# Kernel optimization log

Hardware: AMD Instinct MI355X
Metric: run time of the kernel (lower is better)

Reference implementation:

```python
import jax, jax.numpy as jnp
import numpy as np

L, H, E, V, BS = 12, 12, 768, 50257, 1024
HS = E // H
EPS = 1e-5


def _ln(x, w, b):
    m = jnp.mean(x, axis=-1, keepdims=True)
    v = jnp.mean(jnp.square(x - m), axis=-1, keepdims=True)
    return (x - m) * jax.lax.rsqrt(v + EPS) * w + b


def setup_inputs() -> dict:
    key = jax.random.key(0)
    ks = jax.random.split(key, 16)
    s = 0.02
    inp = {
        "idx": jax.random.randint(ks[0], (2, 1024), 0, V),
        "wte": jax.random.normal(ks[1], (V, E), jnp.float32) * s,
        "wpe": jax.random.normal(ks[2], (BS, E), jnp.float32) * s,
        "ln1_w": jnp.ones((L, E), jnp.float32),
        "ln1_b": jnp.zeros((L, E), jnp.float32),
        "attn_w": jax.random.normal(ks[3], (L, E, 3 * E), jnp.float32) * s,
        "attn_b": jnp.zeros((L, 3 * E), jnp.float32),
        "proj_w": jax.random.normal(ks[4], (L, E, E), jnp.float32) * s,
        "proj_b": jnp.zeros((L, E), jnp.float32),
        "ln2_w": jnp.ones((L, E), jnp.float32),
        "ln2_b": jnp.zeros((L, E), jnp.float32),
        "fc_w": jax.random.normal(ks[5], (L, E, 4 * E), jnp.float32) * s,
        "fc_b": jnp.zeros((L, 4 * E), jnp.float32),
        "fcp_w": jax.random.normal(ks[6], (L, 4 * E, E), jnp.float32) * s,
        "fcp_b": jnp.zeros((L, E), jnp.float32),
        "lnf_w": jnp.ones((E,), jnp.float32),
        "lnf_b": jnp.zeros((E,), jnp.float32),
    }
    return inp


def _gpt_forward(idx, wte, wpe, ln1_w, ln1_b, attn_w, attn_b, proj_w, proj_b,
                 ln2_w, ln2_b, fc_w, fc_b, fcp_w, fcp_b, lnf_w, lnf_b):
    B, T = idx.shape
    x = wte[idx] + wpe[:T]  # [B,T,E]
    causal = jnp.tril(jnp.ones((T, T), bool))
    scale = 1.0 / np.sqrt(HS)

    def block(x, p):
        (l1w, l1b, aw, ab, pw, pb, l2w, l2b, fw, fb, pww, pwb) = p
        qkv = _ln(x, l1w, l1b) @ aw + ab  # [B,T,3E]
        q, k, v = jnp.split(qkv, 3, axis=-1)
        q = q.reshape(B, T, H, HS).transpose(0, 2, 1, 3)  # [B,H,T,hs]
        k = k.reshape(B, T, H, HS).transpose(0, 2, 1, 3)
        v = v.reshape(B, T, H, HS).transpose(0, 2, 1, 3)
        att = jnp.einsum('bhqd,bhkd->bhqk', q, k) * scale
        att = jnp.where(causal, att, -jnp.inf)
        att = jax.nn.softmax(att, axis=-1)
        y = jnp.einsum('bhqk,bhkd->bhqd', att, v)
        y = y.transpose(0, 2, 1, 3).reshape(B, T, E)
        x = x + y @ pw + pb
        h = jax.nn.gelu(_ln(x, l2w, l2b) @ fw + fb, approximate=False)
        x = x + h @ pww + pwb
        return x, None

    params = (ln1_w, ln1_b, attn_w, attn_b, proj_w, proj_b,
              ln2_w, ln2_b, fc_w, fc_b, fcp_w, fcp_b)
    x, _ = jax.lax.scan(block, x, params)
    x = _ln(x, lnf_w, lnf_b)
    return x @ wte.T  # tied lm_head, training-mode full logits [B,T,V]


def reference(idx, wte, wpe, ln1_w, ln1_b, attn_w, attn_b, proj_w, proj_b,
              ln2_w, ln2_b, fc_w, fc_b, fcp_w, fcp_b, lnf_w, lnf_b):
    return _gpt_forward(idx, wte, wpe, ln1_w, ln1_b, attn_w, attn_b, proj_w,
                        proj_b, ln2_w, ln2_b, fc_w, fc_b, fcp_w, fcp_b,
                        lnf_w, lnf_b)
```

## Files before the change

kernel.cpp:

```cpp
#include <hip/hip_runtime.h>
#include <hip/hip_bf16.h>


typedef __bf16 bf16x8 __attribute__((ext_vector_type(8)));
typedef float f32x4 __attribute__((ext_vector_type(4)));
typedef unsigned int u32x4 __attribute__((ext_vector_type(4)));
typedef unsigned short ushort_t;

__device__ inline unsigned short f2bf(float f) {
    unsigned int u = __float_as_uint(f);
    u += 0x7FFFu + ((u >> 16) & 1u);
    return (unsigned short)(u >> 16);
}
__device__ inline unsigned int pk2(float a, float b) {
    return (unsigned int)f2bf(a) | ((unsigned int)f2bf(b) << 16);
}
__device__ inline float gelu_f(float v) {
    return 0.5f * v * (1.0f + erff(v * 0.70710678118654752f));
}
__device__ inline void gld16(const ushort_t* g, ushort_t* l) {
    __builtin_amdgcn_global_load_lds(
        (const __attribute__((address_space(1))) void*)g,
        (__attribute__((address_space(3))) void*)l, 16, 0, 0);
}
__device__ inline void store_c(float* p, float v) { *p = v; }
__device__ inline void store_c(ushort_t* p, float v) { *p = f2bf(v); }

__global__ __launch_bounds__(192) void embed_kernel(
    const int* __restrict__ idx, const float* __restrict__ wte,
    const float* __restrict__ wpe, float* __restrict__ x) {
    int row = blockIdx.x;
    int t = row & 1023;
    int tok = idx[row];
    const float4* src = (const float4*)(wte + (size_t)tok * 768);
    const float4* pe  = (const float4*)(wpe + (size_t)t * 768);
    float4* dst = (float4*)(x + (size_t)row * 768);
    int i = threadIdx.x;
    float4 a = src[i], b = pe[i];
    float4 r; r.x = a.x + b.x; r.y = a.y + b.y; r.z = a.z + b.z; r.w = a.w + b.w;
    dst[i] = r;
}

__device__ inline void ln_body(
    const float* __restrict__ in, const float* __restrict__ w,
    const float* __restrict__ b, ushort_t* __restrict__ out, int row) {
    const float* r = in + (size_t)row * 768;
    int tid = threadIdx.x;
    float v[3];
#pragma unroll
    for (int j = 0; j < 3; j++) v[j] = r[tid + j * 256];
    float s = v[0] + v[1] + v[2];
    __shared__ float sh1[4], sh2[4];
#pragma unroll
    for (int o = 32; o; o >>= 1) s += __shfl_down(s, o);
    if ((tid & 63) == 0) sh1[tid >> 6] = s;
    __syncthreads();
    float mean = (sh1[0] + sh1[1] + sh1[2] + sh1[3]) * (1.0f / 768.0f);
    float d0 = v[0] - mean, d1 = v[1] - mean, d2 = v[2] - mean;
    float sq = d0 * d0 + d1 * d1 + d2 * d2;
#pragma unroll
    for (int o = 32; o; o >>= 1) sq += __shfl_down(sq, o);
    if ((tid & 63) == 0) sh2[tid >> 6] = sq;
    __syncthreads();
    float var = (sh2[0] + sh2[1] + sh2[2] + sh2[3]) * (1.0f / 768.0f);
    float rstd = rsqrtf(var + 1e-5f);
#pragma unroll
    for (int j = 0; j < 3; j++) {
        int c = tid + j * 256;
        out[(size_t)row * 768 + c] = f2bf((v[j] - mean) * rstd * w[c] + b[c]);
    }
}

__global__ __launch_bounds__(256) void ln_kernel(
    const float* __restrict__ in, const float* __restrict__ w,
    const float* __restrict__ b, ushort_t* __restrict__ out) {
    ln_body(in, w, b, out, blockIdx.x);
}

__device__ inline void transpose_tile(
    const float* __restrict__ in, ushort_t* __restrict__ out,
    int N, int K, int n0, int k0) {
    __shared__ float tl[64][65];
    int tid = threadIdx.x;
    int r = tid >> 4, c = (tid & 15) * 4;
#pragma unroll
    for (int j = 0; j < 4; j++) {
        float4 v = *(const float4*)(in + (size_t)(k0 + r + j * 16) * N + n0 + c);
        tl[r + j * 16][c] = v.x; tl[r + j * 16][c + 1] = v.y;
        tl[r + j * 16][c + 2] = v.z; tl[r + j * 16][c + 3] = v.w;
    }
    __syncthreads();
    int nr = tid >> 2, kc = (tid & 3) * 16;
    unsigned int u[8];
#pragma unroll
    for (int j = 0; j < 8; j++)
        u[j] = pk2(tl[kc + 2 * j][nr], tl[kc + 2 * j + 1][nr]);
    u32x4 a = {u[0], u[1], u[2], u[3]}, b = {u[4], u[5], u[6], u[7]};
    ushort_t* op = out + (size_t)(n0 + nr) * K + k0 + kc;
    *(u32x4*)op = a;
    *(u32x4*)(op + 8) = b;
}

__global__ __launch_bounds__(256) void prep1_kernel(
    const float* __restrict__ aw, const float* __restrict__ pw,
    const float* __restrict__ fw, const float* __restrict__ fpw,
    ushort_t* __restrict__ awT, ushort_t* __restrict__ pwT,
    ushort_t* __restrict__ fwT, ushort_t* __restrict__ fpwT,
    const float* __restrict__ x, const float* __restrict__ lw,
    const float* __restrict__ lb, ushort_t* __restrict__ xn) {
    int t = blockIdx.x;
    if (t >= 1728) { ln_body(x, lw, lb, xn, t - 1728); return; }
    const float* in; ushort_t* out; int N, K, n0, k0;
    if (t < 432)       { in = aw;  out = awT;  N = 2304; K = 768;
                         n0 = (t % 36) * 64; k0 = (t / 36) * 64; }
    else if (t < 576)  { t -= 432;  in = pw;  out = pwT;  N = 768;  K = 768;
                         n0 = (t % 12) * 64; k0 = (t / 12) * 64; }
    else if (t < 1152) { t -= 576;  in = fw;  out = fwT;  N = 3072; K = 768;
                         n0 = (t % 48) * 64; k0 = (t / 48) * 64; }
    else               { t -= 1152; in = fpw; out = fpwT; N = 768;  K = 3072;
                         n0 = (t % 12) * 64; k0 = (t / 12) * 64; }
    transpose_tile(in, out, N, K, n0, k0);
}

__global__ __launch_bounds__(256) void convert_bf(
    const float* __restrict__ in, ushort_t* __restrict__ out, long long n8) {
    long long i = (long long)blockIdx.x * 256 + threadIdx.x;
    long long stride = (long long)gridDim.x * 256;
    for (; i < n8; i += stride) {
        const float4* s = (const float4*)(in + i * 8);
        float4 a = s[0], b = s[1];
        u32x4 u = {pk2(a.x, a.y), pk2(a.z, a.w), pk2(b.x, b.y), pk2(b.z, b.w)};
        *(u32x4*)(out + i * 8) = u;
    }
}

__global__ __launch_bounds__(256) void attn_kernel(
    const ushort_t* __restrict__ qkvb,
    const ushort_t* __restrict__ vt,
    ushort_t* __restrict__ y) {
    int qt = (int)gridDim.x - 1 - (int)blockIdx.x;
    int q0 = qt * 128;
    int z = blockIdx.y;
    int b = z / 12, h = z % 12;

    __shared__ __align__(16) ushort_t Ks[64 * 64];
    __shared__ __align__(16) ushort_t Vs[64 * 64];
    __shared__ __align__(16) ushort_t Ps[4][32 * 72];

    int tid = threadIdx.x;
    int lane = tid & 63, w = tid >> 6;
    int fr = lane & 15;
    int g4 = lane >> 4;
    int kg = g4 * 8;

    const ushort_t* qbase = qkvb + (size_t)b * 1024 * 2304;
    bf16x8 qf[2][2];
#pragma unroll
    for (int m = 0; m < 2; m++)
#pragma unroll
        for (int ks = 0; ks < 2; ks++)
            qf[m][ks] = *(const bf16x8*)(qbase +
                (size_t)(q0 + w * 32 + m * 16 + fr) * 2304 + h * 64 + ks * 32 + kg);

    f32x4 oacc[2][4] = {};
    float mrow[2][4], lrow[2][4];
#pragma unroll
    for (int m = 0; m < 2; m++)
#pragma unroll
        for (int i = 0; i < 4; i++) { mrow[m][i] = -1e30f; lrow[m][i] = 0.f; }

    const ushort_t* vtb = vt + (size_t)z * 64 * 1024;
    int nkt = ((q0 + 127) >> 6) + 1;
    const float LOG2E = 1.4426950408889634f;
    const float sc = 0.125f;
    int swr = (fr & 7) << 3;

    for (int kt = 0; kt < nkt; kt++) {
        int k0 = kt << 6;
#pragma unroll
        for (int c2 = 0; c2 < 2; c2++) {
            int c = tid + c2 * 256;
            int row = c >> 3;
            int col8 = ((c & 7) << 3) ^ ((row & 7) << 3);
            gld16(qbase + (size_t)(k0 + row) * 2304 + 768 + h * 64 + col8, Ks + c * 8);
            gld16(vtb + (size_t)row * 1024 + k0 + col8, Vs + c * 8);
        }
        __syncthreads();
        bool active = (k0 <= q0 + w * 32 + 31);
        if (active) {
            f32x4 s[2][4] = {};
#pragma unroll
            for (int ks = 0; ks < 2; ks++) {
                int cc = (ks * 32 + kg) ^ swr;
                bf16x8 kf[4];
#pragma unroll
                for (int n = 0; n < 4; n++)
                    kf[n] = *(const bf16x8*)(Ks + (n * 16 + fr) * 64 + cc);
#pragma unroll
                for (int m = 0; m < 2; m++)
#pragma unroll
                    for (int n = 0; n < 4; n++)
                        s[m][n] = __builtin_amdgcn_mfma_f32_16x16x32_bf16(qf[m][ks], kf[n], s[m][n], 0, 0, 0);
            }
            float al[2][4];
#pragma unroll
            for (int m = 0; m < 2; m++) {
#pragma unroll
                for (int i = 0; i < 4; i++) {
                    int q = q0 + w * 32 + m * 16 + g4 * 4 + i;
                    float pm = -1e30f;
#pragma unroll
                    for (int n = 0; n < 4; n++) {
                        int kv = k0 + n * 16 + fr;
                        float v = (kv <= q) ? s[m][n][i] * sc : -1e30f;
                        s[m][n][i] = v;
                        pm = fmaxf(pm, v);
                    }
                    pm = fmaxf(pm, __shfl_xor(pm, 1));
                    pm = fmaxf(pm, __shfl_xor(pm, 2));
                    pm = fmaxf(pm, __shfl_xor(pm, 4));
                    pm = fmaxf(pm, __shfl_xor(pm, 8));
                    float mn = fmaxf(mrow[m][i], pm);
                    float alpha = __builtin_exp2f((mrow[m][i] - mn) * LOG2E);
                    mrow[m][i] = mn;
                    al[m][i] = alpha;
                    float ps = 0.f;
#pragma unroll
                    for (int n = 0; n < 4; n++) {
                        float pv = __builtin_exp2f((s[m][n][i] - mn) * LOG2E);
                        s[m][n][i] = pv;
                        ps += pv;
                    }
                    ps += __shfl_xor(ps, 1);
                    ps += __shfl_xor(ps, 2);
                    ps += __shfl_xor(ps, 4);
                    ps += __shfl_xor(ps, 8);
                    lrow[m][i] = lrow[m][i] * alpha + ps;
                }
            }
#pragma unroll
            for (int m = 0; m < 2; m++)
#pragma unroll
                for (int nd = 0; nd < 4; nd++)
#pragma unroll
                    for (int i = 0; i < 4; i++)
                        oacc[m][nd][i] *= al[m][i];
#pragma unroll
            for (int m = 0; m < 2; m++)
#pragma unroll
                for (int n = 0; n < 4; n++)
#pragma unroll
                    for (int i = 0; i < 4; i++)
                        Ps[w][(m * 16 + g4 * 4 + i) * 72 + n * 16 + fr] = f2bf(s[m][n][i]);
        }
        __syncthreads();
        if (active) {
#pragma unroll
            for (int ks = 0; ks < 2; ks++) {
                int cc = (ks * 32 + kg) ^ swr;
                bf16x8 pa[2], vf[4];
#pragma unroll
                for (int m = 0; m < 2; m++)
                    pa[m] = *(const bf16x8*)(&Ps[w][(m * 16 + fr) * 72 + ks * 32 + kg]);
#pragma unroll
                for (int nd = 0; nd < 4; nd++)
                    vf[nd] = *(const bf16x8*)(Vs + (nd * 16 + fr) * 64 + cc);
#pragma unroll
                for (int m = 0; m < 2; m++)
#pragma unroll
                    for (int nd = 0; nd < 4; nd++)
                        oacc[m][nd] = __builtin_amdgcn_mfma_f32_16x16x32_bf16(pa[m], vf[nd], oacc[m][nd], 0, 0, 0);
            }
        }
        __syncthreads();
    }
    ushort_t* yb = y + (size_t)b * 1024 * 768 + h * 64;
#pragma unroll
    for (int m = 0; m < 2; m++)
#pragma unroll
        for (int nd = 0; nd < 4; nd++)
#pragma unroll
            for (int i = 0; i < 4; i++) {
                int q = q0 + w * 32 + m * 16 + g4 * 4 + i;
                yb[(size_t)q * 768 + nd * 16 + fr] = f2bf(oacc[m][nd][i] / lrow[m][i]);
            }
}

template <int BM, int EPI, typename TC>
__global__ __launch_bounds__(256) void gemm2(
    const ushort_t* __restrict__ A, int lda,
    const ushort_t* __restrict__ B, int ldb,
    TC* __restrict__ C, int ldc,
    const float* __restrict__ bias, const float* __restrict__ R,
    ushort_t* __restrict__ VT,
    int M, int N, int K) {
    constexpr int MR = BM / 32;
    int brow = blockIdx.y * BM;
    int bcol = blockIdx.x * 128;

    __shared__ __align__(16) ushort_t As[BM * 64];
    __shared__ __align__(16) ushort_t Bs[128 * 64];
    __shared__ __align__(16) ushort_t Tr[EPI == 3 ? 128 * 80 : 1];

    int tid = threadIdx.x;
    int lane = tid & 63, wid = tid >> 6;
    int wr = (wid >> 1) * (BM / 2);
    int wc = (wid & 1) * 64;
    int fr = lane & 15;
    int g4 = lane >> 4;
    int kg = g4 * 8;
    int swr = (fr & 7) << 3;

    int colk = ((tid & 7) << 3) ^ (((tid >> 3) & 7) << 3);
    const ushort_t* Agr[MR];
    const ushort_t* Bgr[4];
#pragma unroll
    for (int rg = 0; rg < MR; rg++)
        Agr[rg] = A + (size_t)(brow + rg * 32 + (tid >> 3)) * lda + colk;
#pragma unroll
    for (int rg = 0; rg < 4; rg++) {
        int br = bcol + rg * 32 + (tid >> 3);
        if (br > N - 1) br = N - 1;
        Bgr[rg] = B + (size_t)br * ldb + colk;
    }
    ushort_t* Al = As + tid * 8;
    ushort_t* Bl = Bs + tid * 8;

    f32x4 acc[MR][4] = {};

    for (int k0 = 0; k0 < K; k0 += 64) {
#pragma unroll
        for (int rg = 0; rg < MR; rg++) gld16(Agr[rg] + k0, Al + rg * 2048);
#pragma unroll
        for (int rg = 0; rg < 4; rg++) gld16(Bgr[rg] + k0, Bl + rg * 2048);
        __syncthreads();
#pragma unroll
        for (int ks = 0; ks < 2; ks++) {
            int cc = (ks * 32 + kg) ^ swr;
            bf16x8 af[MR], bfv[4];
#pragma unroll
            for (int m = 0; m < MR; m++)
                af[m] = *(const bf16x8*)(As + (wr + m * 16 + fr) * 64 + cc);
#pragma unroll
            for (int n = 0; n < 4; n++)
                bfv[n] = *(const bf16x8*)(Bs + (wc + n * 16 + fr) * 64 + cc);
#pragma unroll
            for (int m = 0; m < MR; m++)
#pragma unroll
                for (int n = 0; n < 4; n++)
                    acc[m][n] = __builtin_amdgcn_mfma_f32_16x16x32_bf16(af[m], bfv[n], acc[m][n], 0, 0, 0);
        }
        __syncthreads();
    }

    int cr = g4 * 4;

    if constexpr (EPI == 3) {
        if (bcol >= 1536) {
#pragma unroll
            for (int m = 0; m < MR; m++) {
#pragma unroll
                for (int n = 0; n < 4; n++) {
                    int dl = wc + n * 16 + fr;
                    float bv = bias[bcol + dl];
#pragma unroll
                    for (int i = 0; i < 4; i++) {
                        int tl = wr + m * 16 + cr + i;
                        Tr[dl * 80 + tl] = f2bf(acc[m][n][i] + bv);
                    }
                }
            }
            __syncthreads();
            int bb = brow >> 10, t0g = brow & 1023;
            int dbase = bcol - 1536;
#pragma unroll
            for (int j = 0; j < 4; j++) {
                int lin = tid + j * 256;
                int dl = lin >> 3, t8 = (lin & 7) * 8;
                int dg = dbase + dl;
                int h2 = dg >> 6, dd = dg & 63;
                u32x4 v = *(const u32x4*)&Tr[dl * 80 + t8];
                *(u32x4*)(VT + ((size_t)(bb * 12 + h2) * 64 + dd) * 1024 + t0g + t8) = v;
            }
            return;
        }
    }

#pragma unroll
    for (int m = 0; m < MR; m++) {
#pragma unroll
        for (int n = 0; n < 4; n++) {
            int col = bcol + wc + n * 16 + fr;
            if (col < N) {
                float bv = bias ? bias[col] : 0.0f;
#pragma unroll
                for (int i = 0; i < 4; i++) {
                    int row = brow + wr + m * 16 + cr + i;
                    float v = acc[m][n][i] + bv;
                    if constexpr (EPI == 1) v = gelu_f(v);
                    if constexpr (EPI == 2) v += R[(size_t)row * ldc + col];
                    store_c(&C[(size_t)row * ldc + col], v);
                }
            }
        }
    }
}

__global__ __launch_bounds__(512, 1) void gemm256(
    const ushort_t* __restrict__ A, int lda,
    const ushort_t* __restrict__ B, int ldb,
    float* __restrict__ C, int ldc,
    int M, int N, int K) {
    int Rt = gridDim.x, P = gridDim.y;
    int wgid = blockIdx.x + Rt * blockIdx.y;
    int full = P >> 3;
    int thresh = full * 8 * Rt;
    int r, pp;
    if (wgid < thresh) {
        int g = wgid / (8 * Rt);
        int wi = wgid - g * (8 * Rt);
        r = wi >> 3;
        pp = g * 8 + (wi & 7);
    } else {
        int off = wgid - thresh;
        pp = full * 8 + off / Rt;
        r = off - (off / Rt) * Rt;
    }
    int brow = r * 256;
    int bcol = pp * 256;

    __shared__ __align__(16) ushort_t As[2][256 * 64];
    __shared__ __align__(16) ushort_t Bs[2][256 * 64];

    int tid = threadIdx.x;
    int lane = tid & 63, wid = tid >> 6;
    int wr = (wid >> 2) * 128;
    int wc = (wid & 3) * 64;
    int fr = lane & 15;
    int g4 = lane >> 4;
    int kg = g4 * 8;
    int swr = (fr & 7) << 3;

    int srow = tid >> 3;
    int scol = ((tid & 7) << 3) ^ ((srow & 7) << 3);
    const ushort_t* Ag[4];
    const ushort_t* Bg[4];
#pragma unroll
    for (int s = 0; s < 4; s++) {
        Ag[s] = A + (size_t)(brow + s * 64 + srow) * lda + scol;
        int br = bcol + s * 64 + srow;
        if (br > N - 1) br = N - 1;
        Bg[s] = B + (size_t)br * ldb + scol;
    }

    f32x4 acc[8][4] = {};
    int nt = K >> 6;

#pragma unroll
    for (int s = 0; s < 4; s++) {
        gld16(Ag[s], &As[0][s * 4096 + tid * 8]);
        gld16(Bg[s], &Bs[0][s * 4096 + tid * 8]);
    }

    for (int t = 0; t < nt; t++) {
        int cur = t & 1;
        if (t + 1 < nt) {
            int nxt = cur ^ 1;
            int k0 = (t + 1) << 6;
#pragma unroll
            for (int s = 0; s < 4; s++) {
                gld16(Ag[s] + k0, &As[nxt][s * 4096 + tid * 8]);
                gld16(Bg[s] + k0, &Bs[nxt][s * 4096 + tid * 8]);
            }
            asm volatile("s_waitcnt vmcnt(8)" ::: "memory");
        } else {
            asm volatile("s_waitcnt vmcnt(0)" ::: "memory");
        }
        __builtin_amdgcn_sched_barrier(0);
        __builtin_amdgcn_s_barrier();
        __builtin_amdgcn_sched_barrier(0);

        const ushort_t* Ab = &As[cur][0];
        const ushort_t* Bb = &Bs[cur][0];
#pragma unroll
        for (int ks = 0; ks < 2; ks++) {
            int cc = (ks * 32 + kg) ^ swr;
            bf16x8 af[8], bfv[4];
#pragma unroll
            for (int m = 0; m < 8; m++)
                af[m] = *(const bf16x8*)(Ab + (wr + m * 16 + fr) * 64 + cc);
#pragma unroll
            for (int n = 0; n < 4; n++)
                bfv[n] = *(const bf16x8*)(Bb + (wc + n * 16 + fr) * 64 + cc);
#pragma unroll
            for (int m = 0; m < 8; m++)
#pragma unroll
                for (int n = 0; n < 4; n++)
                    acc[m][n] = __builtin_amdgcn_mfma_f32_16x16x32_bf16(af[m], bfv[n], acc[m][n], 0, 0, 0);
        }
        asm volatile("s_waitcnt lgkmcnt(0)" ::: "memory");
        __builtin_amdgcn_sched_barrier(0);
        __builtin_amdgcn_s_barrier();
        __builtin_amdgcn_sched_barrier(0);
    }

    int cr = g4 * 4;
#pragma unroll
    for (int m = 0; m < 8; m++) {
#pragma unroll
        for (int n = 0; n < 4; n++) {
            int col = bcol + wc + n * 16 + fr;
            if (col < N) {
#pragma unroll
                for (int i = 0; i < 4; i++) {
                    int row = brow + wr + m * 16 + cr + i;
                    C[(size_t)row * ldc + col] = acc[m][n][i];
                }
            }
        }
    }
}

extern "C" void kernel_launch(void* const* d_in, const int* in_sizes, int n_in,
                              void* d_out, int out_size, void* d_ws, size_t ws_size,
                              hipStream_t stream) {
    const int*   idx    = (const int*)d_in[0];
    const float* wte    = (const float*)d_in[1];
    const float* wpe    = (const float*)d_in[2];
    const float* ln1_w  = (const float*)d_in[3];
    const float* ln1_b  = (const float*)d_in[4];
    const float* attn_w = (const float*)d_in[5];
    const float* attn_b = (const float*)d_in[6];
    const float* proj_w = (const float*)d_in[7];
    const float* proj_b = (const float*)d_in[8];
    const float* ln2_w  = (const float*)d_in[9];
    const float* ln2_b  = (const float*)d_in[10];
    const float* fc_w   = (const float*)d_in[11];
    const float* fc_b   = (const float*)d_in[12];
    const float* fcp_w  = (const float*)d_in[13];
    const float* fcp_b  = (const float*)d_in[14];
    const float* lnf_w  = (const float*)d_in[15];
    const float* lnf_b  = (const float*)d_in[16];
    float* out = (float*)d_out;

    char* p = (char*)d_ws;
    float*    x    = (float*)p;    p += (size_t)2048 * 768 * 4;
    ushort_t* xn   = (ushort_t*)p; p += (size_t)2048 * 768 * 2;
    ushort_t* qkvb = (ushort_t*)p; p += (size_t)2048 * 2304 * 2;
    ushort_t* y    = (ushort_t*)p; p += (size_t)2048 * 768 * 2;
    ushort_t* h    = (ushort_t*)p; p += (size_t)2048 * 3072 * 2;
    ushort_t* vt   = (ushort_t*)p; p += (size_t)24 * 64 * 1024 * 2;
    ushort_t* wteb = (ushort_t*)p; p += (size_t)50257 * 768 * 2;
    ushort_t* awT  = (ushort_t*)p; p += (size_t)2304 * 768 * 2;
    ushort_t* pwT  = (ushort_t*)p; p += (size_t)768 * 768 * 2;
    ushort_t* fwT  = (ushort_t*)p; p += (size_t)3072 * 768 * 2;
    ushort_t* fpwT = (ushort_t*)p; p += (size_t)768 * 3072 * 2;

    embed_kernel<<<2048, 192, 0, stream>>>(idx, wte, wpe, x);

    for (int l = 0; l < 12; l++) {
        prep1_kernel<<<3776, 256, 0, stream>>>(
            attn_w + (size_t)l * 768 * 2304, proj_w + (size_t)l * 768 * 768,
            fc_w + (size_t)l * 768 * 3072, fcp_w + (size_t)l * 3072 * 768,
            awT, pwT, fwT, fpwT,
            x, ln1_w + l * 768, ln1_b + l * 768, xn);
        gemm2<64, 3, ushort_t><<<dim3(18, 32), 256, 0, stream>>>(
            xn, 768, awT, 768, qkvb, 2304,
            attn_b + l * 2304, nullptr, vt, 2048, 2304, 768);
        attn_kernel<<<dim3(8, 24), 256, 0, stream>>>(qkvb, vt, y);
        gemm2<64, 2, float><<<dim3(6, 32), 256, 0, stream>>>(
            y, 768, pwT, 768, x, 768,
            proj_b + l * 768, x, nullptr, 2048, 768, 768);
        ln_kernel<<<2048, 256, 0, stream>>>(x, ln2_w + l * 768, ln2_b + l * 768, xn);
        gemm2<64, 1, ushort_t><<<dim3(24, 32), 256, 0, stream>>>(
            xn, 768, fwT, 768, h, 3072,
            fc_b + l * 3072, nullptr, nullptr, 2048, 3072, 768);
        gemm2<64, 2, float><<<dim3(6, 32), 256, 0, stream>>>(
            h, 3072, fpwT, 3072, x, 768,
            fcp_b + l * 768, x, nullptr, 2048, 768, 3072);
    }

    convert_bf<<<4096, 256, 0, stream>>>(wte, wteb, (50257LL * 768) / 8);
    ln_kernel<<<2048, 256, 0, stream>>>(x, lnf_w, lnf_b, xn);
    gemm256<<<dim3(8, 197), 512, 0, stream>>>(
        xn, 768, wteb, 768, out, 50257, 2048, 50257, 768);
}
```

Before: 2.355 ms.

## Double-buffer LDS tiles in per-layer GEMMs with explicit vmcnt waits

Rewrites the layer GEMM kernel so LDS tiles for A and B are double-buffered. The next K-tile's global-to-LDS loads are issued before computing on the current tile, with waitcnt and raw s_barrier in place of __syncthreads. This is meant to hide global load latency behind MFMA work. The FC GEMM also moves to BM=128 with half the row blocks. The cost is doubled LDS use, which may lower occupancy, and the hand-written vmcnt counts depend on the per-thread load count.

```diff
diff --git a/kernel.cpp b/kernel.cpp
--- a/kernel.cpp
+++ b/kernel.cpp
@@ -287,7 +287,7 @@
 }
 
 template <int BM, int EPI, typename TC>
-__global__ __launch_bounds__(256) void gemm2(
+__global__ __launch_bounds__(256) void gemm3(
     const ushort_t* __restrict__ A, int lda,
     const ushort_t* __restrict__ B, int ldb,
     TC* __restrict__ C, int ldc,
@@ -298,8 +298,8 @@
     int brow = blockIdx.y * BM;
     int bcol = blockIdx.x * 128;
 
-    __shared__ __align__(16) ushort_t As[BM * 64];
-    __shared__ __align__(16) ushort_t Bs[128 * 64];
+    __shared__ __align__(16) ushort_t As[2][BM * 64];
+    __shared__ __align__(16) ushort_t Bs[2][128 * 64];
     __shared__ __align__(16) ushort_t Tr[EPI == 3 ? 128 * 80 : 1];
 
     int tid = threadIdx.x;
@@ -311,46 +311,68 @@
     int kg = g4 * 8;
     int swr = (fr & 7) << 3;
 
-    int colk = ((tid & 7) << 3) ^ (((tid >> 3) & 7) << 3);
-    const ushort_t* Agr[MR];
-    const ushort_t* Bgr[4];
-#pragma unroll
-    for (int rg = 0; rg < MR; rg++)
-        Agr[rg] = A + (size_t)(brow + rg * 32 + (tid >> 3)) * lda + colk;
-#pragma unroll
-    for (int rg = 0; rg < 4; rg++) {
-        int br = bcol + rg * 32 + (tid >> 3);
+    int srow = tid >> 3;
+    int scol = ((tid & 7) << 3) ^ ((srow & 7) << 3);
+    const ushort_t* Ag[MR];
+    const ushort_t* Bg[4];
+#pragma unroll
+    for (int s = 0; s < MR; s++)
+        Ag[s] = A + (size_t)(brow + s * 32 + srow) * lda + scol;
+#pragma unroll
+    for (int s = 0; s < 4; s++) {
+        int br = bcol + s * 32 + srow;
         if (br > N - 1) br = N - 1;
-        Bgr[rg] = B + (size_t)br * ldb + colk;
-    }
-    ushort_t* Al = As + tid * 8;
-    ushort_t* Bl = Bs + tid * 8;
+        Bg[s] = B + (size_t)br * ldb + scol;
+    }
 
     f32x4 acc[MR][4] = {};
-
-    for (int k0 = 0; k0 < K; k0 += 64) {
-#pragma unroll
-        for (int rg = 0; rg < MR; rg++) gld16(Agr[rg] + k0, Al + rg * 2048);
-#pragma unroll
-        for (int rg = 0; rg < 4; rg++) gld16(Bgr[rg] + k0, Bl + rg * 2048);
-        __syncthreads();
+    int nt = K >> 6;
+
+#pragma unroll
+    for (int s = 0; s < MR; s++) gld16(Ag[s], &As[0][s * 2048 + tid * 8]);
+#pragma unroll
+    for (int s = 0; s < 4; s++)  gld16(Bg[s], &Bs[0][s * 2048 + tid * 8]);
+
+    for (int t = 0; t < nt; t++) {
+        int cur = t & 1;
+        if (t + 1 < nt) {
+            int nxt = cur ^ 1;
+            int k0 = (t + 1) << 6;
+#pragma unroll
+            for (int s = 0; s < MR; s++) gld16(Ag[s] + k0, &As[nxt][s * 2048 + tid * 8]);
+#pragma unroll
+            for (int s = 0; s < 4; s++)  gld16(Bg[s] + k0, &Bs[nxt][s * 2048 + tid * 8]);
+            if constexpr (MR == 4) asm volatile("s_waitcnt vmcnt(8)" ::: "memory");
+            else                   asm volatile("s_waitcnt vmcnt(6)" ::: "memory");
+        } else {
+            asm volatile("s_waitcnt vmcnt(0)" ::: "memory");
+        }
+        __builtin_amdgcn_sched_barrier(0);
+        __builtin_amdgcn_s_barrier();
+        __builtin_amdgcn_sched_barrier(0);
+
+        const ushort_t* Ab = &As[cur][0];
+        const ushort_t* Bb = &Bs[cur][0];
 #pragma unroll
         for (int ks = 0; ks < 2; ks++) {
             int cc = (ks * 32 + kg) ^ swr;
             bf16x8 af[MR], bfv[4];
 #pragma unroll
             for (int m = 0; m < MR; m++)
-                af[m] = *(const bf16x8*)(As + (wr + m * 16 + fr) * 64 + cc);
+                af[m] = *(const bf16x8*)(Ab + (wr + m * 16 + fr) * 64 + cc);
 #pragma unroll
             for (int n = 0; n < 4; n++)
-                bfv[n] = *(const bf16x8*)(Bs + (wc + n * 16 + fr) * 64 + cc);
+                bfv[n] = *(const bf16x8*)(Bb + (wc + n * 16 + fr) * 64 + cc);
 #pragma unroll
             for (int m = 0; m < MR; m++)
 #pragma unroll
                 for (int n = 0; n < 4; n++)
                     acc[m][n] = __builtin_amdgcn_mfma_f32_16x16x32_bf16(af[m], bfv[n], acc[m][n], 0, 0, 0);
         }
-        __syncthreads();
+        asm volatile("s_waitcnt lgkmcnt(0)" ::: "memory");
+        __builtin_amdgcn_sched_barrier(0);
+        __builtin_amdgcn_s_barrier();
+        __builtin_amdgcn_sched_barrier(0);
     }
 
     int cr = g4 * 4;
@@ -564,18 +586,18 @@
             fc_w + (size_t)l * 768 * 3072, fcp_w + (size_t)l * 3072 * 768,
             awT, pwT, fwT, fpwT,
             x, ln1_w + l * 768, ln1_b + l * 768, xn);
-        gemm2<64, 3, ushort_t><<<dim3(18, 32), 256, 0, stream>>>(
+        gemm3<64, 3, ushort_t><<<dim3(18, 32), 256, 0, stream>>>(
             xn, 768, awT, 768, qkvb, 2304,
             attn_b + l * 2304, nullptr, vt, 2048, 2304, 768);
         attn_kernel<<<dim3(8, 24), 256, 0, stream>>>(qkvb, vt, y);
-        gemm2<64, 2, float><<<dim3(6, 32), 256, 0, stream>>>(
+        gemm3<64, 2, float><<<dim3(6, 32), 256, 0, stream>>>(
             y, 768, pwT, 768, x, 768,
             proj_b + l * 768, x, nullptr, 2048, 768, 768);
         ln_kernel<<<2048, 256, 0, stream>>>(x, ln2_w + l * 768, ln2_b + l * 768, xn);
-        gemm2<64, 1, ushort_t><<<dim3(24, 32), 256, 0, stream>>>(
+        gemm3<128, 1, ushort_t><<<dim3(24, 16), 256, 0, stream>>>(
             xn, 768, fwT, 768, h, 3072,
             fc_b + l * 3072, nullptr, nullptr, 2048, 3072, 768);
-        gemm2<64, 2, float><<<dim3(6, 32), 256, 0, stream>>>(
+        gemm3<64, 2, float><<<dim3(6, 32), 256, 0, stream>>>(
             h, 3072, fpwT, 3072, x, 768,
             fcp_b + l * 768, x, nullptr, 2048, 768, 3072);
     }
```

New measurement: 2.523 ms. +7.2%, slower.

## Narrow lm_head GEMM tile to 256x128 with triple-buffered loads; fuse final LN with wte convert

Applied to the files above, without the earlier changes.

The lm_head GEMM tile shrinks from 256x256 to 256x128, giving 8 waves of 64x64 each and doubling the grid to 393 column tiles. The shared-memory pipeline moves from double to triple buffering, prefetching two k-steps ahead with adjusted vmcnt waits. The final layernorm and the wte fp32-to-bf16 conversion are merged into one launch to drop a kernel boundary. The narrower tile lowers register pressure and improves wave balance, but halves per-wave MFMA reuse and adds A-operand reloads.

```diff
diff --git a/kernel.cpp b/kernel.cpp
--- a/kernel.cpp
+++ b/kernel.cpp
@@ -122,15 +122,20 @@
     transpose_tile(in, out, N, K, n0, k0);
 }
 
-__global__ __launch_bounds__(256) void convert_bf(
-    const float* __restrict__ in, ushort_t* __restrict__ out, long long n8) {
-    long long i = (long long)blockIdx.x * 256 + threadIdx.x;
-    long long stride = (long long)gridDim.x * 256;
+__global__ __launch_bounds__(256) void lnfconv_kernel(
+    const float* __restrict__ x, const float* __restrict__ lw,
+    const float* __restrict__ lb, ushort_t* __restrict__ xn,
+    const float* __restrict__ wte, ushort_t* __restrict__ wteb) {
+    int t = blockIdx.x;
+    if (t < 2048) { ln_body(x, lw, lb, xn, t); return; }
+    const long long n8 = (50257LL * 768) / 8;
+    long long i = (long long)(t - 2048) * 256 + threadIdx.x;
+    long long stride = 4096LL * 256;
     for (; i < n8; i += stride) {
-        const float4* s = (const float4*)(in + i * 8);
+        const float4* s = (const float4*)(wte + i * 8);
         float4 a = s[0], b = s[1];
         u32x4 u = {pk2(a.x, a.y), pk2(a.z, a.w), pk2(b.x, b.y), pk2(b.z, b.w)};
-        *(u32x4*)(out + i * 8) = u;
+        *(u32x4*)(wteb + i * 8) = u;
     }
 }
 
@@ -427,15 +432,15 @@
         r = off - (off / Rt) * Rt;
     }
     int brow = r * 256;
-    int bcol = pp * 256;
-
-    __shared__ __align__(16) ushort_t As[2][256 * 64];
-    __shared__ __align__(16) ushort_t Bs[2][256 * 64];
+    int bcol = pp * 128;
+
+    __shared__ __align__(16) ushort_t As[3][256 * 64];
+    __shared__ __align__(16) ushort_t Bs[3][128 * 64];
 
     int tid = threadIdx.x;
     int lane = tid & 63, wid = tid >> 6;
-    int wr = (wid >> 2) * 128;
-    int wc = (wid & 3) * 64;
+    int wr = (wid >> 1) * 64;
+    int wc = (wid & 1) * 64;
     int fr = lane & 15;
     int g4 = lane >> 4;
     int kg = g4 * 8;
@@ -444,35 +449,41 @@
     int srow = tid >> 3;
     int scol = ((tid & 7) << 3) ^ ((srow & 7) << 3);
     const ushort_t* Ag[4];
-    const ushort_t* Bg[4];
-#pragma unroll
-    for (int s = 0; s < 4; s++) {
+    const ushort_t* Bg[2];
+#pragma unroll
+    for (int s = 0; s < 4; s++)
         Ag[s] = A + (size_t)(brow + s * 64 + srow) * lda + scol;
+#pragma unroll
+    for (int s = 0; s < 2; s++) {
         int br = bcol + s * 64 + srow;
         if (br > N - 1) br = N - 1;
         Bg[s] = B + (size_t)br * ldb + scol;
     }
 
-    f32x4 acc[8][4] = {};
+    f32x4 acc[4][4] = {};
     int nt = K >> 6;
 
 #pragma unroll
-    for (int s = 0; s < 4; s++) {
-        gld16(Ag[s], &As[0][s * 4096 + tid * 8]);
-        gld16(Bg[s], &Bs[0][s * 4096 + tid * 8]);
-    }
+    for (int s = 0; s < 4; s++) gld16(Ag[s], &As[0][s * 4096 + tid * 8]);
+#pragma unroll
+    for (int s = 0; s < 2; s++) gld16(Bg[s], &Bs[0][s * 4096 + tid * 8]);
+#pragma unroll
+    for (int s = 0; s < 4; s++) gld16(Ag[s] + 64, &As[1][s * 4096 + tid * 8]);
+#pragma unroll
+    for (int s = 0; s < 2; s++) gld16(Bg[s] + 64, &Bs[1][s * 4096 + tid * 8]);
 
     for (int t = 0; t < nt; t++) {
-        int cur = t & 1;
-        if (t + 1 < nt) {
-            int nxt = cur ^ 1;
-            int k0 = (t + 1) << 6;
-#pragma unroll
-            for (int s = 0; s < 4; s++) {
-                gld16(Ag[s] + k0, &As[nxt][s * 4096 + tid * 8]);
-                gld16(Bg[s] + k0, &Bs[nxt][s * 4096 + tid * 8]);
-            }
-            asm volatile("s_waitcnt vmcnt(8)" ::: "memory");
+        int cur = t % 3;
+        if (t + 2 < nt) {
+            int nxt = (t + 2) % 3;
+            int k0 = (t + 2) << 6;
+#pragma unroll
+            for (int s = 0; s < 4; s++) gld16(Ag[s] + k0, &As[nxt][s * 4096 + tid * 8]);
+#pragma unroll
+            for (int s = 0; s < 2; s++) gld16(Bg[s] + k0, &Bs[nxt][s * 4096 + tid * 8]);
+            asm volatile("s_waitcnt vmcnt(12)" ::: "memory");
+        } else if (t + 1 < nt) {
+            asm volatile("s_waitcnt vmcnt(6)" ::: "memory");
         } else {
             asm volatile("s_waitcnt vmcnt(0)" ::: "memory");
         }
@@ -485,15 +496,15 @@
 #pragma unroll
         for (int ks = 0; ks < 2; ks++) {
             int cc = (ks * 32 + kg) ^ swr;
-            bf16x8 af[8], bfv[4];
-#pragma unroll
-            for (int m = 0; m < 8; m++)
+            bf16x8 af[4], bfv[4];
+#pragma unroll
+            for (int m = 0; m < 4; m++)
                 af[m] = *(const bf16x8*)(Ab + (wr + m * 16 + fr) * 64 + cc);
 #pragma unroll
             for (int n = 0; n < 4; n++)
                 bfv[n] = *(const bf16x8*)(Bb + (wc + n * 16 + fr) * 64 + cc);
 #pragma unroll
-            for (int m = 0; m < 8; m++)
+            for (int m = 0; m < 4; m++)
 #pragma unroll
                 for (int n = 0; n < 4; n++)
                     acc[m][n] = __builtin_amdgcn_mfma_f32_16x16x32_bf16(af[m], bfv[n], acc[m][n], 0, 0, 0);
@@ -506,7 +517,7 @@
 
     int cr = g4 * 4;
 #pragma unroll
-    for (int m = 0; m < 8; m++) {
+    for (int m = 0; m < 4; m++) {
 #pragma unroll
         for (int n = 0; n < 4; n++) {
             int col = bcol + wc + n * 16 + fr;
@@ -580,8 +591,7 @@
             fcp_b + l * 768, x, nullptr, 2048, 768, 3072);
     }
 
-    convert_bf<<<4096, 256, 0, stream>>>(wte, wteb, (50257LL * 768) / 8);
-    ln_kernel<<<2048, 256, 0, stream>>>(x, lnf_w, lnf_b, xn);
-    gemm256<<<dim3(8, 197), 512, 0, stream>>>(
+    lnfconv_kernel<<<6144, 256, 0, stream>>>(x, lnf_w, lnf_b, xn, wte, wteb);
+    gemm256<<<dim3(8, 393), 512, 0, stream>>>(
         xn, 768, wteb, 768, out, 50257, 2048, 50257, 768);
 }
```

Result: slower. 2.410 ms (+2.4%).

## Double-buffer weight transposes and overlap next layer's prep with attention

Applied to the files above, without the earlier changes.

The per-layer weight transpose/convert is taken out of the kernel that also ran LN1. It now goes into double-buffered bf16 weight buffers, and the next layer's transposes run as extra blocks inside the attention kernel. The attention kernel launches only 192 blocks, so the spare CUs can do that work instead of it sitting serially before the QKV GEMM. The first layer's transposes are folded into the embedding kernel, and the final LN is merged with the wte bf16 conversion. The cost is an extra set of weight buffers in the workspace and a separate LN1 launch.

```diff
diff --git a/kernel.cpp b/kernel.cpp
--- a/kernel.cpp
+++ b/kernel.cpp
@@ -25,21 +25,6 @@
 }
 __device__ inline void store_c(float* p, float v) { *p = v; }
 __device__ inline void store_c(ushort_t* p, float v) { *p = f2bf(v); }
-
-__global__ __launch_bounds__(192) void embed_kernel(
-    const int* __restrict__ idx, const float* __restrict__ wte,
-    const float* __restrict__ wpe, float* __restrict__ x) {
-    int row = blockIdx.x;
-    int t = row & 1023;
-    int tok = idx[row];
-    const float4* src = (const float4*)(wte + (size_t)tok * 768);
-    const float4* pe  = (const float4*)(wpe + (size_t)t * 768);
-    float4* dst = (float4*)(x + (size_t)row * 768);
-    int i = threadIdx.x;
-    float4 a = src[i], b = pe[i];
-    float4 r; r.x = a.x + b.x; r.y = a.y + b.y; r.z = a.z + b.z; r.w = a.w + b.w;
-    dst[i] = r;
-}
 
 __device__ inline void ln_body(
     const float* __restrict__ in, const float* __restrict__ w,
@@ -101,46 +86,73 @@
     *(u32x4*)(op + 8) = b;
 }
 
-__global__ __launch_bounds__(256) void prep1_kernel(
+__device__ inline void transpose_dispatch(
+    int t,
     const float* __restrict__ aw, const float* __restrict__ pw,
     const float* __restrict__ fw, const float* __restrict__ fpw,
     ushort_t* __restrict__ awT, ushort_t* __restrict__ pwT,
-    ushort_t* __restrict__ fwT, ushort_t* __restrict__ fpwT,
+    ushort_t* __restrict__ fwT, ushort_t* __restrict__ fpwT) {
+    if (t < 432)       transpose_tile(aw,  awT,  2304, 768, (t % 36) * 64, (t / 36) * 64);
+    else if (t < 576)  { t -= 432;  transpose_tile(pw,  pwT,  768,  768, (t % 12) * 64, (t / 12) * 64); }
+    else if (t < 1152) { t -= 576;  transpose_tile(fw,  fwT,  3072, 768, (t % 48) * 64, (t / 48) * 64); }
+    else               { t -= 1152; transpose_tile(fpw, fpwT, 768, 3072, (t % 12) * 64, (t / 12) * 64); }
+}
+
+__global__ __launch_bounds__(256) void embed0_kernel(
+    const int* __restrict__ idx, const float* __restrict__ wte,
+    const float* __restrict__ wpe, float* __restrict__ x,
+    const float* __restrict__ aw, const float* __restrict__ pw,
+    const float* __restrict__ fw, const float* __restrict__ fpw,
+    ushort_t* __restrict__ awT, ushort_t* __restrict__ pwT,
+    ushort_t* __restrict__ fwT, ushort_t* __restrict__ fpwT) {
+    int t = blockIdx.x;
+    if (t < 2048) {
+        int row = t, tt = row & 1023;
+        int tok = idx[row];
+        int tid = threadIdx.x;
+#pragma unroll
+        for (int j = 0; j < 3; j++) {
+            int c = tid + j * 256;
+            x[(size_t)row * 768 + c] = wte[(size_t)tok * 768 + c] + wpe[(size_t)tt * 768 + c];
+        }
+        return;
+    }
+    transpose_dispatch(t - 2048, aw, pw, fw, fpw, awT, pwT, fwT, fpwT);
+}
+
+__global__ __launch_bounds__(256) void lnfconv_kernel(
     const float* __restrict__ x, const float* __restrict__ lw,
-    const float* __restrict__ lb, ushort_t* __restrict__ xn) {
+    const float* __restrict__ lb, ushort_t* __restrict__ xn,
+    const float* __restrict__ wte, ushort_t* __restrict__ wteb) {
     int t = blockIdx.x;
-    if (t >= 1728) { ln_body(x, lw, lb, xn, t - 1728); return; }
-    const float* in; ushort_t* out; int N, K, n0, k0;
-    if (t < 432)       { in = aw;  out = awT;  N = 2304; K = 768;
-                         n0 = (t % 36) * 64; k0 = (t / 36) * 64; }
-    else if (t < 576)  { t -= 432;  in = pw;  out = pwT;  N = 768;  K = 768;
-                         n0 = (t % 12) * 64; k0 = (t / 12) * 64; }
-    else if (t < 1152) { t -= 576;  in = fw;  out = fwT;  N = 3072; K = 768;
-                         n0 = (t % 48) * 64; k0 = (t / 48) * 64; }
-    else               { t -= 1152; in = fpw; out = fpwT; N = 768;  K = 3072;
-                         n0 = (t % 12) * 64; k0 = (t / 12) * 64; }
-    transpose_tile(in, out, N, K, n0, k0);
-}
-
-__global__ __launch_bounds__(256) void convert_bf(
-    const float* __restrict__ in, ushort_t* __restrict__ out, long long n8) {
-    long long i = (long long)blockIdx.x * 256 + threadIdx.x;
-    long long stride = (long long)gridDim.x * 256;
+    if (t < 2048) { ln_body(x, lw, lb, xn, t); return; }
+    const long long n8 = (50257LL * 768) / 8;
+    long long i = (long long)(t - 2048) * 256 + threadIdx.x;
+    long long stride = 4096LL * 256;
     for (; i < n8; i += stride) {
-        const float4* s = (const float4*)(in + i * 8);
+        const float4* s = (const float4*)(wte + i * 8);
         float4 a = s[0], b = s[1];
         u32x4 u = {pk2(a.x, a.y), pk2(a.z, a.w), pk2(b.x, b.y), pk2(b.z, b.w)};
-        *(u32x4*)(out + i * 8) = u;
-    }
-}
-
-__global__ __launch_bounds__(256) void attn_kernel(
+        *(u32x4*)(wteb + i * 8) = u;
+    }
+}
+
+__global__ __launch_bounds__(256) void attn_tr_kernel(
     const ushort_t* __restrict__ qkvb,
     const ushort_t* __restrict__ vt,
-    ushort_t* __restrict__ y) {
-    int qt = (int)gridDim.x - 1 - (int)blockIdx.x;
+    ushort_t* __restrict__ y,
+    const float* __restrict__ aw, const float* __restrict__ pw,
+    const float* __restrict__ fw, const float* __restrict__ fpw,
+    ushort_t* __restrict__ awT, ushort_t* __restrict__ pwT,
+    ushort_t* __restrict__ fwT, ushort_t* __restrict__ fpwT) {
+    if (blockIdx.x >= 192) {
+        transpose_dispatch(blockIdx.x - 192, aw, pw, fw, fpw, awT, pwT, fwT, fpwT);
+        return;
+    }
+    int bid = blockIdx.x;
+    int qt = 7 - (bid & 7);
     int q0 = qt * 128;
-    int z = blockIdx.y;
+    int z = bid >> 3;
     int b = z / 12, h = z % 12;
 
     __shared__ __align__(16) ushort_t Ks[64 * 64];
@@ -543,6 +555,9 @@
     const float* lnf_b  = (const float*)d_in[16];
     float* out = (float*)d_out;
 
+    const size_t S_AW = (size_t)2304 * 768, S_PW = (size_t)768 * 768;
+    const size_t S_FW = (size_t)3072 * 768, S_FPW = (size_t)768 * 3072;
+
     char* p = (char*)d_ws;
     float*    x    = (float*)p;    p += (size_t)2048 * 768 * 4;
     ushort_t* xn   = (ushort_t*)p; p += (size_t)2048 * 768 * 2;
@@ -551,37 +566,43 @@
     ushort_t* h    = (ushort_t*)p; p += (size_t)2048 * 3072 * 2;
     ushort_t* vt   = (ushort_t*)p; p += (size_t)24 * 64 * 1024 * 2;
     ushort_t* wteb = (ushort_t*)p; p += (size_t)50257 * 768 * 2;
-    ushort_t* awT  = (ushort_t*)p; p += (size_t)2304 * 768 * 2;
-    ushort_t* pwT  = (ushort_t*)p; p += (size_t)768 * 768 * 2;
-    ushort_t* fwT  = (ushort_t*)p; p += (size_t)3072 * 768 * 2;
-    ushort_t* fpwT = (ushort_t*)p; p += (size_t)768 * 3072 * 2;
-
-    embed_kernel<<<2048, 192, 0, stream>>>(idx, wte, wpe, x);
+    ushort_t* awT[2], *pwT[2], *fwT[2], *fpwT[2];
+    for (int i = 0; i < 2; i++) {
+        awT[i]  = (ushort_t*)p; p += S_AW * 2;
+        pwT[i]  = (ushort_t*)p; p += S_PW * 2;
+        fwT[i]  = (ushort_t*)p; p += S_FW * 2;
+        fpwT[i] = (ushort_t*)p; p += S_FPW * 2;
+    }
+
+    embed0_kernel<<<3776, 256, 0, stream>>>(
+        idx, wte, wpe, x,
+        attn_w, proj_w, fc_w, fcp_w, awT[0], pwT[0], fwT[0], fpwT[0]);
 
     for (int l = 0; l < 12; l++) {
-        prep1_kernel<<<3776, 256, 0, stream>>>(
-            attn_w + (size_t)l * 768 * 2304, proj_w + (size_t)l * 768 * 768,
-            fc_w + (size_t)l * 768 * 3072, fcp_w + (size_t)l * 3072 * 768,
-            awT, pwT, fwT, fpwT,
-            x, ln1_w + l * 768, ln1_b + l * 768, xn);
+        int cb = l & 1, nb = cb ^ 1;
+        ln_kernel<<<2048, 256, 0, stream>>>(x, ln1_w + l * 768, ln1_b + l * 768, xn);
         gemm2<64, 3, ushort_t><<<dim3(18, 32), 256, 0, stream>>>(
-            xn, 768, awT, 768, qkvb, 2304,
+            xn, 768, awT[cb], 768, qkvb, 2304,
             attn_b + l * 2304, nullptr, vt, 2048, 2304, 768);
-        attn_kernel<<<dim3(8, 24), 256, 0, stream>>>(qkvb, vt, y);
+        int nblk = (l < 11) ? 1920 : 192;
+        attn_tr_kernel<<<nblk, 256, 0, stream>>>(
+            qkvb, vt, y,
+            attn_w + (size_t)(l + 1) * S_AW, proj_w + (size_t)(l + 1) * S_PW,
+            fc_w + (size_t)(l + 1) * S_FW, fcp_w + (size_t)(l + 1) * S_FPW,
+            awT[nb], pwT[nb], fwT[nb], fpwT[nb]);
         gemm2<64, 2, float><<<dim3(6, 32), 256, 0, stream>>>(
-            y, 768, pwT, 768, x, 768,
+            y, 768, pwT[cb], 768, x, 768,
             proj_b + l * 768, x, nullptr, 2048, 768, 768);
         ln_kernel<<<2048, 256, 0, stream>>>(x, ln2_w + l * 768, ln2_b + l * 768, xn);
         gemm2<64, 1, ushort_t><<<dim3(24, 32), 256, 0, stream>>>(
-            xn, 768, fwT, 768, h, 3072,
+            xn, 768, fwT[cb], 768, h, 3072,
             fc_b + l * 3072, nullptr, nullptr, 2048, 3072, 768);
         gemm2<64, 2, float><<<dim3(6, 32), 256, 0, stream>>>(
-            h, 3072, fpwT, 3072, x, 768,
+            h, 3072, fpwT[cb], 3072, x, 768,
             fcp_b + l * 768, x, nullptr, 2048, 768, 3072);
     }
 
-    convert_bf<<<4096, 256, 0, stream>>>(wte, wteb, (50257LL * 768) / 8);
-    ln_kernel<<<2048, 256, 0, stream>>>(x, lnf_w, lnf_b, xn);
+    lnfconv_kernel<<<6144, 256, 0, stream>>>(x, lnf_w, lnf_b, xn, wte, wteb);
     gemm256<<<dim3(8, 197), 512, 0, stream>>>(
         xn, 768, wteb, 768, out, 50257, 2048, 50257, 768);
 }
```

Measured after the change: 2.264 ms (median of 3 runs). -3.8%, faster.
